# Kernel tuning notes

Measured on AMD Instinct MI355X. Metric: run time of the kernel, lower is better.

Reference implementation:

```python
import jax, jax.numpy as jnp
import numpy as np

HID = 3584
NH = 16
NKV = 8
HD = 256
T = 2048
THETA = 10000.0
SCALE = 256.0 ** -0.5          # query_pre_attn_scalar ** -0.5
SOFT_CAP = 50.0                # Gemma2 attn_logits_soft_cap


def setup_inputs() -> dict:
    key = jax.random.key(0)
    k1, k2, k3 = jax.random.split(key, 3)
    return {
        "positions": jnp.arange(T, dtype=jnp.int32),
        "hidden_states": jax.random.normal(k1, (T, HID), dtype=jnp.float32),
        "w_qkv": jax.random.normal(k2, (HID, (NH + 2 * NKV) * HD), dtype=jnp.float32) * 0.02,
        "w_o": jax.random.normal(k3, (NH * HD, HID), dtype=jnp.float32) * 0.02,
    }


def _apply_rope(x, positions):
    # neox-style rotary embedding over full head_dim
    d = x.shape[-1]
    inv_freq = 1.0 / (THETA ** (jnp.arange(0, d, 2, dtype=jnp.float32) / d))  # [d/2]
    freqs = positions.astype(jnp.float32)[:, None] * inv_freq[None, :]        # [T, d/2]
    cos = jnp.concatenate([jnp.cos(freqs)] * 2, axis=-1)[:, None, :]          # [T,1,d]
    sin = jnp.concatenate([jnp.sin(freqs)] * 2, axis=-1)[:, None, :]
    x1, x2 = jnp.split(x, 2, axis=-1)
    rotated = jnp.concatenate([-x2, x1], axis=-1)
    return x * cos + rotated * sin


def reference(positions, hidden_states, w_qkv, w_o):
    t = hidden_states.shape[0]
    qkv = hidden_states @ w_qkv                                   # [T, (NH+2*NKV)*HD]
    q = qkv[:, : NH * HD].reshape(t, NH, HD)
    k = qkv[:, NH * HD:(NH + NKV) * HD].reshape(t, NKV, HD)
    v = qkv[:, (NH + NKV) * HD:].reshape(t, NKV, HD)

    q = _apply_rope(q, positions)
    k = _apply_rope(k, positions)

    rep = NH // NKV                                               # GQA expansion
    k = jnp.repeat(k, rep, axis=1)                                # [T, NH, HD]
    v = jnp.repeat(v, rep, axis=1)

    scores = jnp.einsum("qhd,khd->hqk", q, k) * SCALE             # [NH, T, T]
    scores = SOFT_CAP * jnp.tanh(scores / SOFT_CAP)               # logit soft-cap
    causal = jnp.tril(jnp.ones((t, t), dtype=bool))
    scores = jnp.where(causal[None, :, :], scores, -jnp.inf)
    probs = jax.nn.softmax(scores, axis=-1)
    out = jnp.einsum("hqk,khd->qhd", probs, v).reshape(t, NH * HD)
    return out @ w_o                                              # [T, HID]
```

## Files before the change

### kernel.cpp

```cpp
#include <hip/hip_runtime.h>
#include <hip/hip_bf16.h>


#define T_SEQ 2048
#define HID_DIM 3584
#define NH 16
#define NKV 8
#define HD 256
#define QKV_N ((NH + 2 * NKV) * HD)
#define ATT_N (NH * HD)
#define V_OFF ((NH + NKV) * HD)

typedef __bf16 bf16_t;
typedef bf16_t bf16x8 __attribute__((ext_vector_type(8)));
typedef float f32x4 __attribute__((ext_vector_type(4)));

__device__ __forceinline__ void gload16(const bf16_t* g, bf16_t* l) {
  __builtin_amdgcn_global_load_lds(
      (const __attribute__((address_space(1))) unsigned int*)g,
      (__attribute__((address_space(3))) unsigned int*)l, 16, 0, 0);
}

__global__ __launch_bounds__(256) void convert_bf16(
    const float* __restrict__ in, bf16_t* __restrict__ out) {
  const long i = ((long)blockIdx.x * 256 + threadIdx.x) * 8;
  const float4 f0 = *(const float4*)(in + i);
  const float4 f1 = *(const float4*)(in + i + 4);
  bf16x8 v;
  v[0] = (bf16_t)f0.x; v[1] = (bf16_t)f0.y; v[2] = (bf16_t)f0.z; v[3] = (bf16_t)f0.w;
  v[4] = (bf16_t)f1.x; v[5] = (bf16_t)f1.y; v[6] = (bf16_t)f1.z; v[7] = (bf16_t)f1.w;
  *(bf16x8*)(out + i) = v;
}

__global__ __launch_bounds__(256) void transpose_bf16(
    const float* __restrict__ in, bf16_t* __restrict__ out, int K, int N) {
  __shared__ __align__(16) bf16_t tile[64][80];
  const int k0 = blockIdx.x * 64;
  const int n0 = blockIdx.y * 64;
  const int t = threadIdx.x;
  const int rr = t >> 4;
  const int rc = (t & 15) * 4;
#pragma unroll
  for (int i = 0; i < 4; ++i) {
    const int k = rr + i * 16;
    const float4 v = *(const float4*)(in + (long)(k0 + k) * N + n0 + rc);
    tile[rc + 0][k] = (bf16_t)v.x;
    tile[rc + 1][k] = (bf16_t)v.y;
    tile[rc + 2][k] = (bf16_t)v.z;
    tile[rc + 3][k] = (bf16_t)v.w;
  }
  __syncthreads();
  const int wn = t >> 3;
  const int wk = (t & 7) * 8;
#pragma unroll
  for (int i = 0; i < 2; ++i) {
    const int n = wn + i * 32;
    *(bf16x8*)(out + (long)(n0 + n) * K + k0 + wk) = *(const bf16x8*)&tile[n][wk];
  }
}

template <typename TC>
__global__ __launch_bounds__(256) void gemm_bt(
    const bf16_t* __restrict__ A, const bf16_t* __restrict__ Bt,
    TC* __restrict__ C, bf16_t* __restrict__ Vt, int voff,
    int M, int N, int K) {
  const int n0 = blockIdx.x * 128;
  const int m0 = blockIdx.y * 128;
  const int t = threadIdx.x;
  const int w = t >> 6;
  const int lane = t & 63;
  const int l16 = lane & 15;
  const int quad = lane >> 4;

  __shared__ __align__(16) bf16_t As[128][32];
  __shared__ __align__(16) bf16_t Bs[128][32];

  f32x4 acc[4][4];
#pragma unroll
  for (int i = 0; i < 4; ++i)
#pragma unroll
    for (int j = 0; j < 4; ++j) acc[i][j] = f32x4{0, 0, 0, 0};

  const int srow = lane >> 2;
  const int scol = (lane & 3) * 8;
  const bf16_t* gsrc;
  bf16_t* lbase;
  if (w < 2) {
    gsrc = A + (long)(m0 + w * 64 + srow) * K + scol;
    lbase = &As[w * 64][0];
  } else {
    gsrc = Bt + (long)(n0 + (w - 2) * 64 + srow) * K + scol;
    lbase = &Bs[(w - 2) * 64][0];
  }

  const int wm = w & 1;
  const int wn = w >> 1;

  for (int k0 = 0; k0 < K; k0 += 32) {
#pragma unroll
    for (int j = 0; j < 4; ++j)
      gload16(gsrc + (long)j * 16 * K + k0, lbase + j * (16 * 32));
    __syncthreads();

    bf16x8 af[4], bfr[4];
#pragma unroll
    for (int i = 0; i < 4; ++i) {
      af[i] = *(const bf16x8*)&As[wm * 64 + i * 16 + l16][quad * 8];
      bfr[i] = *(const bf16x8*)&Bs[wn * 64 + i * 16 + l16][quad * 8];
    }
#pragma unroll
    for (int i = 0; i < 4; ++i)
#pragma unroll
      for (int j = 0; j < 4; ++j)
        acc[i][j] = __builtin_amdgcn_mfma_f32_16x16x32_bf16(af[i], bfr[j],
                                                            acc[i][j], 0, 0, 0);
    __syncthreads();
  }

#pragma unroll
  for (int i = 0; i < 4; ++i) {
    const int row = m0 + wm * 64 + i * 16 + quad * 4;
#pragma unroll
    for (int j = 0; j < 4; ++j) {
      const int col = n0 + wn * 64 + j * 16 + l16;
#pragma unroll
      for (int r = 0; r < 4; ++r) {
        if (col >= voff)
          Vt[(long)(col - voff) * QKV_N + (row + r)] = (bf16_t)acc[i][j][r];
        else
          C[(long)(row + r) * N + col] = (TC)acc[i][j][r];
      }
    }
  }
}

__global__ void rope_kernel(const int* __restrict__ positions,
                            bf16_t* __restrict__ qkv) {
  const int head = blockIdx.x;
  const int trow = blockIdx.y;
  const int d = threadIdx.x;
  const long col0 = (head < NH) ? (long)head * HD
                                : (long)(NH * HD) + (long)(head - NH) * HD;
  bf16_t* p = qkv + (long)trow * QKV_N + col0;
  const float pos = (float)positions[trow];
  const float inv_freq = exp2f(-(float)d * (13.287712379549449f / 128.0f));
  const float ang = pos * inv_freq;
  float s, c;
  sincosf(ang, &s, &c);
  const float x1 = (float)p[d];
  const float x2 = (float)p[d + 128];
  p[d]       = (bf16_t)(x1 * c - x2 * s);
  p[d + 128] = (bf16_t)(x2 * c + x1 * s);
}

__global__ __launch_bounds__(256) void attn_mfma(
    const bf16_t* __restrict__ qkv, const bf16_t* __restrict__ vt,
    bf16_t* __restrict__ out ) {
  const int lid = blockIdx.x;
  const int kvh = lid & 7;
  const int slot = lid >> 3;
  const int h = 2 * kvh + (slot & 1);
  const int chunk = 127 - (slot >> 1);
  const int q0 = chunk * 16;
  const int ktiles = (chunk >> 1) + 1;
  const int t = threadIdx.x;
  const int w = t >> 6;
  const int lane = t & 63;
  const int l16 = lane & 15;
  const int quad = lane >> 4;
  const int base = ktiles >> 2;
  const int rem = ktiles & 3;
  const int cnt = base + (w < rem ? 1 : 0);
  const int start = w * base + (w < rem ? w : rem);

  __shared__ __align__(16) bf16_t Ps[4][16][40];
  __shared__ float sm[4][16], sl[4][16];
  __shared__ __align__(16) float slabA[16][260];
  __shared__ __align__(16) float slabB[16][260];

  bf16x8 qf[8];
  const bf16_t* qbase = qkv + (long)(q0 + l16) * QKV_N + h * HD + quad * 8;
#pragma unroll
  for (int s = 0; s < 8; ++s) qf[s] = *(const bf16x8*)(qbase + s * 32);

  const bf16_t* kbase = qkv + (long)l16 * QKV_N + (NH * HD) + kvh * HD + quad * 8;
  const bf16_t* vbase = vt + (long)(kvh * HD + l16) * QKV_N + quad * 8;

  f32x4 oacc[16];
#pragma unroll
  for (int nt = 0; nt < 16; ++nt) oacc[nt] = f32x4{0, 0, 0, 0};
  float m_state[4], l_state[4];
#pragma unroll
  for (int r = 0; r < 4; ++r) { m_state[r] = -1e30f; l_state[r] = 0.0f; }

  for (int kt = start; kt < start + cnt; ++kt) {
    bf16x8 kf[2][8];
    const bf16_t* kp = kbase + (long)(kt * 32) * QKV_N;
#pragma unroll
    for (int g = 0; g < 2; ++g)
#pragma unroll
      for (int s = 0; s < 8; ++s)
        kf[g][s] = *(const bf16x8*)(kp + (long)(g * 16) * QKV_N + s * 32);

    f32x4 sacc[2] = {f32x4{0, 0, 0, 0}, f32x4{0, 0, 0, 0}};
    __builtin_amdgcn_s_setprio(1);
#pragma unroll
    for (int g = 0; g < 2; ++g)
#pragma unroll
      for (int s = 0; s < 8; ++s)
        sacc[g] = __builtin_amdgcn_mfma_f32_16x16x32_bf16(qf[s], kf[g][s],
                                                          sacc[g], 0, 0, 0);
    __builtin_amdgcn_s_setprio(0);

    float alpha[4];
#pragma unroll
    for (int r = 0; r < 4; ++r) {
      const int row = q0 + quad * 4 + r;
      float svg[2];
      float best = -1e30f;
#pragma unroll
      for (int g = 0; g < 2; ++g) {
        const float x = sacc[g][r] * 0.0625f;
        const float e = __expf(x * 0.04f);
        const float tz = 50.0f * (e - 1.0f) / (e + 1.0f);
        const int col = kt * 32 + g * 16 + l16;
        svg[g] = (col <= row) ? tz : -1e30f;
        best = fmaxf(best, svg[g]);
      }
      best = fmaxf(best, __shfl_xor(best, 1));
      best = fmaxf(best, __shfl_xor(best, 2));
      best = fmaxf(best, __shfl_xor(best, 4));
      best = fmaxf(best, __shfl_xor(best, 8));
      const float mnew = fmaxf(m_state[r], best);
      float psum = 0.0f;
#pragma unroll
      for (int g = 0; g < 2; ++g) {
        const float pv = (svg[g] > -1e29f) ? __expf(svg[g] - mnew) : 0.0f;
        Ps[w][quad * 4 + r][g * 16 + l16] = (bf16_t)pv;
        psum += pv;
      }
      psum += __shfl_xor(psum, 1);
      psum += __shfl_xor(psum, 2);
      psum += __shfl_xor(psum, 4);
      psum += __shfl_xor(psum, 8);
      alpha[r] = __expf(m_state[r] - mnew);
      l_state[r] = l_state[r] * alpha[r] + psum;
      m_state[r] = mnew;
    }
#pragma unroll
    for (int nt = 0; nt < 16; ++nt) {
      oacc[nt][0] *= alpha[0];
      oacc[nt][1] *= alpha[1];
      oacc[nt][2] *= alpha[2];
      oacc[nt][3] *= alpha[3];
    }

    const bf16x8 pa = *(const bf16x8*)&Ps[w][l16][quad * 8];

#pragma unroll
    for (int h2 = 0; h2 < 2; ++h2) {
      bf16x8 vf[8];
#pragma unroll
      for (int nt = 0; nt < 8; ++nt)
        vf[nt] = *(const bf16x8*)(vbase + (long)(h2 * 128 + nt * 16) * QKV_N +
                                  kt * 32);
      __builtin_amdgcn_s_setprio(1);
#pragma unroll
      for (int nt = 0; nt < 8; ++nt)
        oacc[h2 * 8 + nt] = __builtin_amdgcn_mfma_f32_16x16x32_bf16(
            pa, vf[nt], oacc[h2 * 8 + nt], 0, 0, 0);
      __builtin_amdgcn_s_setprio(0);
    }
  }

  if (l16 == 0) {
#pragma unroll
    for (int r = 0; r < 4; ++r) {
      sm[w][quad * 4 + r] = m_state[r];
      sl[w][quad * 4 + r] = l_state[r];
    }
  }
  __syncthreads();

  float fac[4], lsum[4];
#pragma unroll
  for (int r = 0; r < 4; ++r) {
    const int row = quad * 4 + r;
    const float mstar = fmaxf(fmaxf(sm[0][row], sm[1][row]),
                              fmaxf(sm[2][row], sm[3][row]));
    fac[r] = __expf(m_state[r] - mstar);
    float ls = 0.0f;
#pragma unroll
    for (int j = 0; j < 4; ++j) ls += __expf(sm[j][row] - mstar) * sl[j][row];
    lsum[r] = ls;
  }
#pragma unroll
  for (int nt = 0; nt < 16; ++nt) {
    oacc[nt][0] *= fac[0];
    oacc[nt][1] *= fac[1];
    oacc[nt][2] *= fac[2];
    oacc[nt][3] *= fac[3];
  }

  if (w == 1 || w == 3) {
    float(*slab)[260] = (w == 1) ? slabA : slabB;
#pragma unroll
    for (int r = 0; r < 4; ++r)
#pragma unroll
      for (int nt = 0; nt < 16; ++nt)
        slab[quad * 4 + r][nt * 16 + l16] = oacc[nt][r];
  }
  __syncthreads();
  if (w == 0) {
#pragma unroll
    for (int r = 0; r < 4; ++r)
#pragma unroll
      for (int nt = 0; nt < 16; ++nt)
        oacc[nt][r] += slabA[quad * 4 + r][nt * 16 + l16];
  } else if (w == 2) {
#pragma unroll
    for (int r = 0; r < 4; ++r)
#pragma unroll
      for (int nt = 0; nt < 16; ++nt)
        oacc[nt][r] += slabB[quad * 4 + r][nt * 16 + l16];
  }
  __syncthreads();
  if (w == 2) {
#pragma unroll
    for (int r = 0; r < 4; ++r)
#pragma unroll
      for (int nt = 0; nt < 16; ++nt)
        slabA[quad * 4 + r][nt * 16 + l16] = oacc[nt][r];
  }
  __syncthreads();
  if (w == 0) {
#pragma unroll
    for (int r = 0; r < 4; ++r) {
      const float inv = 1.0f / lsum[r];
      bf16_t* op = out + (long)(q0 + quad * 4 + r) * ATT_N + h * HD + l16;
#pragma unroll
      for (int nt = 0; nt < 16; ++nt)
        op[nt * 16] =
            (bf16_t)((oacc[nt][r] + slabA[quad * 4 + r][nt * 16 + l16]) * inv);
    }
  }
}

extern "C" void kernel_launch(void* const* d_in, const int* in_sizes, int n_in,
                              void* d_out, int out_size, void* d_ws, size_t ws_size,
                              hipStream_t stream) {
  const int* positions = (const int*)d_in[0];
  const float* hidden = (const float*)d_in[1];
  const float* w_qkv = (const float*)d_in[2];
  const float* w_o = (const float*)d_in[3];
  float* out = (float*)d_out;

  bf16_t* qkv = (bf16_t*)d_ws;
  bf16_t* attn = qkv + (size_t)T_SEQ * QKV_N;
  bf16_t* hid_bf = attn + (size_t)T_SEQ * ATT_N;
  bf16_t* wqkv_t = hid_bf + (size_t)T_SEQ * HID_DIM;
  bf16_t* wo_t = wqkv_t + (size_t)QKV_N * HID_DIM;
  bf16_t* vtb = qkv + V_OFF;

  convert_bf16<<<(T_SEQ * HID_DIM) / 2048, 256, 0, stream>>>(hidden, hid_bf);
  transpose_bf16<<<dim3(HID_DIM / 64, QKV_N / 64), 256, 0, stream>>>(
      w_qkv, wqkv_t, HID_DIM, QKV_N);
  transpose_bf16<<<dim3(ATT_N / 64, HID_DIM / 64), 256, 0, stream>>>(
      w_o, wo_t, ATT_N, HID_DIM);

  gemm_bt<bf16_t><<<dim3(QKV_N / 128, T_SEQ / 128), 256, 0, stream>>>(
      hid_bf, wqkv_t, qkv, vtb, V_OFF, T_SEQ, QKV_N, HID_DIM);
  rope_kernel<<<dim3(NH + NKV, T_SEQ), 128, 0, stream>>>(positions, qkv);
  attn_mfma<<<2048, 256, 0, stream>>>(qkv, vtb, attn);
  gemm_bt<float><<<dim3(HID_DIM / 128, T_SEQ / 128), 256, 0, stream>>>(
      attn, wo_t, out, attn , 1 << 30, T_SEQ, HID_DIM, ATT_N);
}
```

Baseline: 843.4 us.

## Use soft-cap bound as fixed softmax max and compute row sums via MFMA

Because the soft-cap limits every logit to at most 50, the kernel now uses 50 as a fixed softmax maximum. Each probability becomes a single exp2 of a reciprocal, and the online max, the shuffle reductions, the per-tile rescaling of the output accumulator and the cross-wave max merge are all removed. Row sums are accumulated with an extra MFMA against a vector of ones, and all V fragments are loaded before the softmax so their latency overlaps with it. Launch bounds now request one block per SM. The trade-off is less precision headroom: probabilities are scaled by up to exp(-100), which can push very negative rows toward the fp32/bf16 denormal range.

Result: no change. 838.8 us (-0.6%).

```diff
diff --git a/kernel.cpp b/kernel.cpp
--- a/kernel.cpp
+++ b/kernel.cpp
@@ -153,7 +153,7 @@
   p[d + 128] = (bf16_t)(x2 * c + x1 * s);
 }
 
-__global__ __launch_bounds__(256) void attn_mfma(
+__global__ __launch_bounds__(256, 1) void attn_mfma(
     const bf16_t* __restrict__ qkv, const bf16_t* __restrict__ vt,
     bf16_t* __restrict__ out ) {
   const int lid = blockIdx.x;
@@ -174,10 +174,13 @@
   const int start = w * base + (w < rem ? w : rem);
 
   __shared__ __align__(16) bf16_t Ps[4][16][40];
-  __shared__ float sm[4][16], sl[4][16];
+  __shared__ float sl[4][16];
   __shared__ __align__(16) float slabA[16][260];
   __shared__ __align__(16) float slabB[16][260];
 
+  const float C1 = 0.0036067376022224085f;
+  const float C2 = -144.26950408889634f;
+
   bf16x8 qf[8];
   const bf16_t* qbase = qkv + (long)(q0 + l16) * QKV_N + h * HD + quad * 8;
 #pragma unroll
@@ -186,12 +189,14 @@
   const bf16_t* kbase = qkv + (long)l16 * QKV_N + (NH * HD) + kvh * HD + quad * 8;
   const bf16_t* vbase = vt + (long)(kvh * HD + l16) * QKV_N + quad * 8;
 
+  bf16x8 onesf;
+#pragma unroll
+  for (int j = 0; j < 8; ++j) onesf[j] = (bf16_t)1.0f;
+
   f32x4 oacc[16];
 #pragma unroll
   for (int nt = 0; nt < 16; ++nt) oacc[nt] = f32x4{0, 0, 0, 0};
-  float m_state[4], l_state[4];
-#pragma unroll
-  for (int r = 0; r < 4; ++r) { m_state[r] = -1e30f; l_state[r] = 0.0f; }
+  f32x4 lacc = f32x4{0, 0, 0, 0};
 
   for (int kt = start; kt < start + cnt; ++kt) {
     bf16x8 kf[2][8];
@@ -212,94 +217,49 @@
                                                           sacc[g], 0, 0, 0);
     __builtin_amdgcn_s_setprio(0);
 
-    float alpha[4];
+    bf16x8 vf[16];
+    {
+      const bf16_t* vp = vbase + kt * 32;
+#pragma unroll
+      for (int nt = 0; nt < 16; ++nt)
+        vf[nt] = *(const bf16x8*)(vp + (long)(nt * 16) * QKV_N);
+    }
+
 #pragma unroll
     for (int r = 0; r < 4; ++r) {
       const int row = q0 + quad * 4 + r;
-      float svg[2];
-      float best = -1e30f;
 #pragma unroll
       for (int g = 0; g < 2; ++g) {
-        const float x = sacc[g][r] * 0.0625f;
-        const float e = __expf(x * 0.04f);
-        const float tz = 50.0f * (e - 1.0f) / (e + 1.0f);
+        const float e2 = exp2f(sacc[g][r] * C1);
+        float p = exp2f(C2 * __builtin_amdgcn_rcpf(e2 + 1.0f));
         const int col = kt * 32 + g * 16 + l16;
-        svg[g] = (col <= row) ? tz : -1e30f;
-        best = fmaxf(best, svg[g]);
+        p = (col <= row) ? p : 0.0f;
+        Ps[w][quad * 4 + r][g * 16 + l16] = (bf16_t)p;
       }
-      best = fmaxf(best, __shfl_xor(best, 1));
-      best = fmaxf(best, __shfl_xor(best, 2));
-      best = fmaxf(best, __shfl_xor(best, 4));
-      best = fmaxf(best, __shfl_xor(best, 8));
-      const float mnew = fmaxf(m_state[r], best);
-      float psum = 0.0f;
-#pragma unroll
-      for (int g = 0; g < 2; ++g) {
-        const float pv = (svg[g] > -1e29f) ? __expf(svg[g] - mnew) : 0.0f;
-        Ps[w][quad * 4 + r][g * 16 + l16] = (bf16_t)pv;
-        psum += pv;
-      }
-      psum += __shfl_xor(psum, 1);
-      psum += __shfl_xor(psum, 2);
-      psum += __shfl_xor(psum, 4);
-      psum += __shfl_xor(psum, 8);
-      alpha[r] = __expf(m_state[r] - mnew);
-      l_state[r] = l_state[r] * alpha[r] + psum;
-      m_state[r] = mnew;
-    }
-#pragma unroll
-    for (int nt = 0; nt < 16; ++nt) {
-      oacc[nt][0] *= alpha[0];
-      oacc[nt][1] *= alpha[1];
-      oacc[nt][2] *= alpha[2];
-      oacc[nt][3] *= alpha[3];
     }
 
     const bf16x8 pa = *(const bf16x8*)&Ps[w][l16][quad * 8];
 
-#pragma unroll
-    for (int h2 = 0; h2 < 2; ++h2) {
-      bf16x8 vf[8];
-#pragma unroll
-      for (int nt = 0; nt < 8; ++nt)
-        vf[nt] = *(const bf16x8*)(vbase + (long)(h2 * 128 + nt * 16) * QKV_N +
-                                  kt * 32);
-      __builtin_amdgcn_s_setprio(1);
-#pragma unroll
-      for (int nt = 0; nt < 8; ++nt)
-        oacc[h2 * 8 + nt] = __builtin_amdgcn_mfma_f32_16x16x32_bf16(
-            pa, vf[nt], oacc[h2 * 8 + nt], 0, 0, 0);
-      __builtin_amdgcn_s_setprio(0);
-    }
+    __builtin_amdgcn_s_setprio(1);
+    lacc = __builtin_amdgcn_mfma_f32_16x16x32_bf16(pa, onesf, lacc, 0, 0, 0);
+#pragma unroll
+    for (int nt = 0; nt < 16; ++nt)
+      oacc[nt] = __builtin_amdgcn_mfma_f32_16x16x32_bf16(pa, vf[nt],
+                                                         oacc[nt], 0, 0, 0);
+    __builtin_amdgcn_s_setprio(0);
   }
 
   if (l16 == 0) {
 #pragma unroll
-    for (int r = 0; r < 4; ++r) {
-      sm[w][quad * 4 + r] = m_state[r];
-      sl[w][quad * 4 + r] = l_state[r];
-    }
-  }
-  __syncthreads();
-
-  float fac[4], lsum[4];
+    for (int r = 0; r < 4; ++r) sl[w][quad * 4 + r] = lacc[r];
+  }
+  __syncthreads();
+
+  float lsum[4];
 #pragma unroll
   for (int r = 0; r < 4; ++r) {
     const int row = quad * 4 + r;
-    const float mstar = fmaxf(fmaxf(sm[0][row], sm[1][row]),
-                              fmaxf(sm[2][row], sm[3][row]));
-    fac[r] = __expf(m_state[r] - mstar);
-    float ls = 0.0f;
-#pragma unroll
-    for (int j = 0; j < 4; ++j) ls += __expf(sm[j][row] - mstar) * sl[j][row];
-    lsum[r] = ls;
-  }
-#pragma unroll
-  for (int nt = 0; nt < 16; ++nt) {
-    oacc[nt][0] *= fac[0];
-    oacc[nt][1] *= fac[1];
-    oacc[nt][2] *= fac[2];
-    oacc[nt][3] *= fac[3];
+    lsum[r] = (sl[0][row] + sl[1][row]) + (sl[2][row] + sl[3][row]);
   }
 
   if (w == 1 || w == 3) {
```
